# Performance work log

Hardware: AMD Instinct MI355X
Metric: run time of the kernel (lower is better)

Reference implementation:

```python
import jax, jax.numpy as jnp
import numpy as np
from jax import lax

VOCAB = 32000
EMB = 512
HID = 512
NLAYERS = 2


def _lstm_cell(x, h, c, Wih, Whh, bih, bhh):
    # x:[N,in], h,c:[N,H]; torch gate order i,f,g,o
    z = x @ Wih.T + h @ Whh.T + bih + bhh  # [N,4H]
    i, f, g, o = jnp.split(z, 4, axis=-1)
    c_new = jax.nn.sigmoid(f) * c + jax.nn.sigmoid(i) * jnp.tanh(g)
    h_new = jax.nn.sigmoid(o) * jnp.tanh(c_new)
    return h_new, c_new


def _run_encoder(x_seq, Wih, Whh, bih, bhh):
    # x_seq:[T,N,E]; stacked per-layer weights Wih:[L,4H,in], Whh:[L,4H,H]
    N = x_seq.shape[1]
    H = Whh.shape[-1]
    hs, cs = [], []
    for l in range(Wih.shape[0]):
        h0 = jnp.zeros((N, H), x_seq.dtype)
        c0 = jnp.zeros((N, H), x_seq.dtype)

        def step(carry, x, l=l):
            h, c = carry
            h, c = _lstm_cell(x, h, c, Wih[l], Whh[l], bih[l], bhh[l])
            return (h, c), h

        (hL, cL), x_seq = lax.scan(step, (h0, c0), x_seq)
        hs.append(hL)
        cs.append(cL)
    return jnp.stack(hs), jnp.stack(cs)  # [L,N,H] each


def setup_inputs() -> dict:
    key = jax.random.key(0)
    ks = jax.random.split(key, 16)
    s = 0.05
    inp = {
        "src": jax.random.randint(ks[0], (64, 64), 0, VOCAB),
        "tgt": jax.random.randint(ks[1], (32, 64), 0, VOCAB),
        "enc_emb": jax.random.normal(ks[2], (VOCAB, EMB), jnp.float32) * s,
        "enc_Wih": jax.random.normal(ks[3], (NLAYERS, 4 * HID, EMB), jnp.float32) * s,
        "enc_Whh": jax.random.normal(ks[4], (NLAYERS, 4 * HID, HID), jnp.float32) * s,
        "enc_bih": jax.random.normal(ks[5], (NLAYERS, 4 * HID), jnp.float32) * s,
        "enc_bhh": jax.random.normal(ks[6], (NLAYERS, 4 * HID), jnp.float32) * s,
        "dec_emb": jax.random.normal(ks[7], (VOCAB, EMB), jnp.float32) * s,
        "dec_Wih": jax.random.normal(ks[8], (NLAYERS, 4 * HID, EMB), jnp.float32) * s,
        "dec_Whh": jax.random.normal(ks[9], (NLAYERS, 4 * HID, HID), jnp.float32) * s,
        "dec_bih": jax.random.normal(ks[10], (NLAYERS, 4 * HID), jnp.float32) * s,
        "dec_bhh": jax.random.normal(ks[11], (NLAYERS, 4 * HID), jnp.float32) * s,
        "fc_W": jax.random.normal(ks[12], (VOCAB, HID), jnp.float32) * s,
        "fc_b": jax.random.normal(ks[13], (VOCAB,), jnp.float32) * s,
    }
    return inp


def reference(src, tgt, enc_emb, enc_Wih, enc_Whh, enc_bih, enc_bhh,
              dec_emb, dec_Wih, dec_Whh, dec_bih, dec_bhh, fc_W, fc_b):
    tgt_len, batch = tgt.shape
    # Encoder: embed src then 2-layer LSTM; final (h, c) seeds the decoder.
    src_emb = enc_emb[src]  # [T,N,E] (dropout is identity at p-eval)
    h, c = _run_encoder(src_emb, enc_Wih, enc_Whh, enc_bih, enc_bhh)

    def dec_step(carry, _):
        inp, h, c = carry  # inp:[N] int, h/c:[L,N,H]
        x = dec_emb[inp]  # [N,E]
        hs, cs = [], []
        for l in range(NLAYERS):
            hn, cn = _lstm_cell(x, h[l], c[l], dec_Wih[l], dec_Whh[l],
                                dec_bih[l], dec_bhh[l])
            hs.append(hn)
            cs.append(cn)
            x = hn
        pred = x @ fc_W.T + fc_b  # [N,V]
        nxt = jnp.argmax(pred, axis=-1)  # greedy feedback (ratio=0)
        return (nxt, jnp.stack(hs), jnp.stack(cs)), pred

    init = (tgt[0], h, c)
    _, preds = lax.scan(dec_step, init, None, length=tgt_len - 1)  # [T-1,N,V]
    outputs = jnp.concatenate(
        [jnp.zeros((1, batch, fc_W.shape[0]), preds.dtype), preds], axis=0)
    return outputs[None]  # [B=1, tgt_len, batch, vocab]
```

## Files before the change

kernel.cpp:

```cpp
#include <hip/hip_runtime.h>
#include <cmath>

#define NBLK 256
#define NTHR 512
#define SMEM_BYTES 137216

struct Args {
  const int* src; const int* tgt;
  const float* enc_emb;
  const float* enc_Wih; const float* enc_Whh; const float* enc_bih; const float* enc_bhh;
  const float* dec_emb;
  const float* dec_Wih; const float* dec_Whh; const float* dec_bih; const float* dec_bhh;
  const float* fc_W; const float* fc_b;
  float* out;
  unsigned* bar;
  unsigned long long* gkeys;
  float* hT0[2]; float* hT1[2];
  float* hnm;
  float* seqT;
  float* fcWT;
  int use_wt;
};

__device__ __forceinline__ void gbar(unsigned* bar) {
  __syncthreads();
  if (threadIdx.x == 0) {
    unsigned* gen = bar + 128;
    unsigned g = __hip_atomic_load(gen, __ATOMIC_RELAXED, __HIP_MEMORY_SCOPE_AGENT);
    __hip_atomic_fetch_add(bar + (blockIdx.x & 7) * 16, 1u, __ATOMIC_RELEASE,
                           __HIP_MEMORY_SCOPE_AGENT);
    if (blockIdx.x == 0) {
      unsigned long long target = (unsigned long long)(g + 1) * NBLK;
      for (;;) {
        unsigned long long tot = 0;
#pragma unroll
        for (int i = 0; i < 8; ++i)
          tot += __hip_atomic_load(bar + i * 16, __ATOMIC_RELAXED,
                                   __HIP_MEMORY_SCOPE_AGENT);
        if (tot >= target) break;
      }
      __builtin_amdgcn_fence(__ATOMIC_ACQUIRE, "agent");
      __hip_atomic_fetch_add(gen, 1u, __ATOMIC_RELEASE, __HIP_MEMORY_SCOPE_AGENT);
    } else {
      while (__hip_atomic_load(gen, __ATOMIC_RELAXED, __HIP_MEMORY_SCOPE_AGENT) == g)
        __builtin_amdgcn_s_sleep(1);
      __builtin_amdgcn_fence(__ATOMIC_ACQUIRE, "agent");
    }
  }
  __syncthreads();
}

__device__ __forceinline__ float sigm(float x) { return 1.f / (1.f + expf(-x)); }

__device__ __forceinline__ unsigned long long packkey(float v, int j) {
  unsigned u = __float_as_uint(v);
  u = (u & 0x80000000u) ? ~u : (u | 0x80000000u);
  return ((unsigned long long)u << 32) |
         (unsigned long long)(0xFFFFFFFFu - (unsigned)j);
}

__device__ __forceinline__ unsigned long long umaxll(unsigned long long a,
                                                     unsigned long long b) {
  return a > b ? a : b;
}

__device__ __forceinline__ void fma4(float x, float4 w, float* acc) {
  acc[0] = fmaf(x, w.x, acc[0]); acc[1] = fmaf(x, w.y, acc[1]);
  acc[2] = fmaf(x, w.z, acc[2]); acc[3] = fmaf(x, w.w, acc[3]);
}

__device__ void load_w(float* wlds, float* blds, int rbase,
                       const float* __restrict__ Wih, const float* __restrict__ Whh,
                       const float* __restrict__ bih, const float* __restrict__ bhh)
{
  const int tid = threadIdx.x, bid = blockIdx.x;
  for (int idx = tid; idx < 8 * 256; idx += NTHR) {
    const int r = idx >> 8, c = idx & 255;
    const int j = (r >> 1) * 512 + bid * 2 + (r & 1);
    float4 v;
    if (c < 128) v = *(const float4*)(Wih + (size_t)j * 512 + c * 4);
    else         v = *(const float4*)(Whh + (size_t)j * 512 + (c - 128) * 4);
    *(float4*)(wlds + (size_t)(rbase + r) * 1024 + c * 4) = v;
  }
  if (tid < 8) {
    const int j = (tid >> 1) * 512 + bid * 2 + (tid & 1);
    blds[rbase + tid] = bih[j] + bhh[j];
  }
}

__device__ void fill_tok(unsigned* toklds, const int* __restrict__ idx,
                         const unsigned long long* __restrict__ gkeys)
{
  if (threadIdx.x < 64) {
    unsigned row;
    if (idx) {
      row = (unsigned)idx[threadIdx.x];
    } else {
      unsigned long long best = gkeys[threadIdx.x];
#pragma unroll
      for (int i = 1; i < 8; ++i) best = umaxll(best, gkeys[i * 64 + threadIdx.x]);
      row = 0xFFFFFFFFu - (unsigned)best;
    }
    toklds[threadIdx.x] = row;
  }
  __syncthreads();
}

__device__ void cell(int gather, const float* __restrict__ xsrc,
                     const float* __restrict__ hT_rd, float* __restrict__ hT_wr,
                     int wrow0, float* __restrict__ cl,
                     float* __restrict__ seqT_out, float* __restrict__ hnm_out,
                     const float* __restrict__ wlds, const float* __restrict__ blds,
                     float* __restrict__ tiles, float* __restrict__ zbuf,
                     const unsigned* __restrict__ toklds)
{
  const int tid = threadIdx.x;
  const int lane = tid & 63, wv = tid >> 6;
  const int gate = wv & 3, kh = wv >> 2;
  const int r0 = gate * 2, r1 = r0 + 1;
  const float* wb0 = wlds + (size_t)(wrow0 + r0) * 1024 + kh * 512;
  const float* wb1 = wlds + (size_t)(wrow0 + r1) * 1024 + kh * 512;
  float a0 = 0.f, a1 = 0.f, e0 = 0.f, e1 = 0.f;
  float4 rg0, rg1, rg2, rg3;

  auto load_iter = [&](int it) {
    if (gather) {
      unsigned row = toklds[lane];
      const float* er = xsrc + (size_t)row * 512 + it * 64 + wv * 8;
      rg0 = *(const float4*)er;
      rg1 = *(const float4*)(er + 4);
      const float* hs = hT_rd + it * 4096 + wv * 512 + lane * 4;
      rg2 = *(const float4*)hs;
      rg3 = *(const float4*)(hs + 256);
    } else {
      const float* s = (wv < 4) ? (xsrc + it * 4096 + wv * 1024 + lane * 4)
                                : (hT_rd + it * 4096 + (wv - 4) * 1024 + lane * 4);
      rg0 = *(const float4*)s;
      rg1 = *(const float4*)(s + 256);
      rg2 = *(const float4*)(s + 512);
      rg3 = *(const float4*)(s + 768);
    }
  };
  auto commit_iter = [&](int buf) {
    float* tb = tiles + buf * 8192;
    if (gather) {
      float* tx = tb + (wv * 8) * 64 + lane;
      tx[0]   = rg0.x; tx[64]  = rg0.y; tx[128] = rg0.z; tx[192] = rg0.w;
      tx[256] = rg1.x; tx[320] = rg1.y; tx[384] = rg1.z; tx[448] = rg1.w;
      float* th = tb + 4096 + wv * 512 + lane * 4;
      *(float4*)th = rg2;
      *(float4*)(th + 256) = rg3;
    } else {
      float* t0 = tb + wv * 1024 + lane * 4;
      *(float4*)t0 = rg0;
      *(float4*)(t0 + 256) = rg1;
      *(float4*)(t0 + 512) = rg2;
      *(float4*)(t0 + 768) = rg3;
    }
  };

  load_iter(0);
  commit_iter(0);
#pragma unroll 1
  for (int it = 0; it < 8; ++it) {
    __syncthreads();
    if (it < 7) load_iter(it + 1);
    const float* w0 = wb0 + it * 64;
    const float* w1 = wb1 + it * 64;
    const float* tp = tiles + (it & 1) * 8192 + kh * 4096 + lane;
#pragma unroll
    for (int kk = 0; kk < 64; kk += 4) {
      float4 c0 = *(const float4*)(w0 + kk);
      float4 c1 = *(const float4*)(w1 + kk);
      float x0 = tp[(kk + 0) * 64], x1 = tp[(kk + 1) * 64];
      float x2 = tp[(kk + 2) * 64], x3 = tp[(kk + 3) * 64];
      a0 = fmaf(x0, c0.x, a0); e0 = fmaf(x1, c0.y, e0);
      a0 = fmaf(x2, c0.z, a0); e0 = fmaf(x3, c0.w, e0);
      a1 = fmaf(x0, c1.x, a1); e1 = fmaf(x1, c1.y, e1);
      a1 = fmaf(x2, c1.z, a1); e1 = fmaf(x3, c1.w, e1);
    }
    if (it < 7) commit_iter((it + 1) & 1);
  }
  zbuf[kh * 512 + r0 * 64 + lane] = a0 + e0;
  zbuf[kh * 512 + r1 * 64 + lane] = a1 + e1;
  __syncthreads();
  if (tid < 128) {
    const int mloc = tid >> 6, n = tid & 63;
    float z[4];
#pragma unroll
    for (int g = 0; g < 4; ++g) {
      const int r = g * 2 + mloc;
      z[g] = zbuf[r * 64 + n] + zbuf[512 + r * 64 + n] + blds[wrow0 + r];
    }
    float ig = sigm(z[0]), fg = sigm(z[1]);
    float gg = tanhf(z[2]), og = sigm(z[3]);
    const int m = blockIdx.x * 2 + mloc;
    float cc = fg * cl[mloc * 64 + n] + ig * gg;
    cl[mloc * 64 + n] = cc;
    float hh = og * tanhf(cc);
    hT_wr[m * 64 + n] = hh;
    if (seqT_out) seqT_out[m * 64 + n] = hh;
    if (hnm_out) hnm_out[n * 512 + m] = hh;
  }
}

__device__ void fc_phase(unsigned long long* skeys, int d,
                         const float* __restrict__ h,
                         const float* __restrict__ fcW,
                         const float* __restrict__ fcWT, int use_wt,
                         const float* __restrict__ fcb,
                         float* __restrict__ out,
                         unsigned long long* __restrict__ gkeys, int do_arg)
{
  const int tid = threadIdx.x, bid = blockIdx.x;
  if (do_arg && tid < 64) skeys[tid] = 0ULL;
  __syncthreads();
  if (bid < 250) {
    const int jt = tid & 31, nt = tid >> 5;
    const int j0 = bid * 128 + jt * 4;
    const int n0 = nt * 4;
    float acc[4][4] = {};
    if (use_wt) {
      const float* wt = fcWT + j0;
#pragma unroll 2
      for (int k = 0; k < 512; k += 8) {
        float4 wv[8];
#pragma unroll
        for (int i = 0; i < 8; ++i)
          wv[i] = *(const float4*)(wt + (size_t)(k + i) * 32000);
        float4 ha[4], hb[4];
#pragma unroll
        for (int ni = 0; ni < 4; ++ni) {
          ha[ni] = *(const float4*)(h + (size_t)(n0 + ni) * 512 + k);
          hb[ni] = *(const float4*)(h + (size_t)(n0 + ni) * 512 + k + 4);
        }
#pragma unroll
        for (int ni = 0; ni < 4; ++ni) {
          fma4(ha[ni].x, wv[0], acc[ni]); fma4(ha[ni].y, wv[1], acc[ni]);
          fma4(ha[ni].z, wv[2], acc[ni]); fma4(ha[ni].w, wv[3], acc[ni]);
          fma4(hb[ni].x, wv[4], acc[ni]); fma4(hb[ni].y, wv[5], acc[ni]);
          fma4(hb[ni].z, wv[6], acc[ni]); fma4(hb[ni].w, wv[7], acc[ni]);
        }
      }
    } else {
#pragma unroll 2
      for (int k = 0; k < 512; k += 8) {
        float4 wr[4][2];
#pragma unroll
        for (int i = 0; i < 4; ++i) {
          wr[i][0] = *(const float4*)(fcW + (size_t)(j0 + i) * 512 + k);
          wr[i][1] = *(const float4*)(fcW + (size_t)(j0 + i) * 512 + k + 4);
        }
        float4 ha[4], hb[4];
#pragma unroll
        for (int ni = 0; ni < 4; ++ni) {
          ha[ni] = *(const float4*)(h + (size_t)(n0 + ni) * 512 + k);
          hb[ni] = *(const float4*)(h + (size_t)(n0 + ni) * 512 + k + 4);
        }
#pragma unroll
        for (int ni = 0; ni < 4; ++ni) {
#pragma unroll
          for (int ji = 0; ji < 4; ++ji) {
            float s = acc[ni][ji];
            s = fmaf(ha[ni].x, wr[ji][0].x, s); s = fmaf(ha[ni].y, wr[ji][0].y, s);
            s = fmaf(ha[ni].z, wr[ji][0].z, s); s = fmaf(ha[ni].w, wr[ji][0].w, s);
            s = fmaf(hb[ni].x, wr[ji][1].x, s); s = fmaf(hb[ni].y, wr[ji][1].y, s);
            s = fmaf(hb[ni].z, wr[ji][1].z, s); s = fmaf(hb[ni].w, wr[ji][1].w, s);
            acc[ni][ji] = s;
          }
        }
      }
    }
    const float b0 = fcb[j0], b1 = fcb[j0 + 1], b2 = fcb[j0 + 2], b3 = fcb[j0 + 3];
#pragma unroll
    for (int ni = 0; ni < 4; ++ni) {
      const int n = n0 + ni;
      float4 v = make_float4(acc[ni][0] + b0, acc[ni][1] + b1,
                             acc[ni][2] + b2, acc[ni][3] + b3);
      *(float4*)(out + ((size_t)(d + 1) * 64 + n) * 32000 + j0) = v;
      if (do_arg) {
        unsigned long long kb = umaxll(umaxll(packkey(v.x, j0), packkey(v.y, j0 + 1)),
                                       umaxll(packkey(v.z, j0 + 2), packkey(v.w, j0 + 3)));
        atomicMax(&skeys[n], kb);
      }
    }
  }
  __syncthreads();
  if (do_arg && bid < 250 && tid < 64)
    atomicMax(&gkeys[(bid & 7) * 64 + tid], skeys[tid]);
}

__global__ void __launch_bounds__(256) fc_transpose(const float* __restrict__ W,
                                                    float* __restrict__ WT)
{
  __shared__ float tile[64][65];
  const int jb = blockIdx.x * 64;
  const int kb = blockIdx.y * 64;
  const int t = threadIdx.x;
  const int row = t >> 2, seg = t & 3;
  const float* src = W + (size_t)(jb + row) * 512 + kb + seg * 16;
#pragma unroll
  for (int i = 0; i < 4; ++i) {
    float4 v = *(const float4*)(src + i * 4);
    tile[row][seg * 16 + i * 4 + 0] = v.x;
    tile[row][seg * 16 + i * 4 + 1] = v.y;
    tile[row][seg * 16 + i * 4 + 2] = v.z;
    tile[row][seg * 16 + i * 4 + 3] = v.w;
  }
  __syncthreads();
  float* dst = WT + (size_t)(kb + row) * 32000 + jb + seg * 16;
#pragma unroll
  for (int i = 0; i < 4; ++i) {
    float4 v = make_float4(tile[seg * 16 + i * 4 + 0][row], tile[seg * 16 + i * 4 + 1][row],
                           tile[seg * 16 + i * 4 + 2][row], tile[seg * 16 + i * 4 + 3][row]);
    *(float4*)(dst + i * 4) = v;
  }
}

extern "C" __global__ void __launch_bounds__(NTHR, 2)
s2s_main(Args a)
{
  extern __shared__ float smem[];
  float* wlds  = smem;
  float* tiles = wlds + 16384;
  float* zbuf  = tiles + 16384;
  float* blds  = zbuf + 1024;
  float* clds  = blds + 16;
  unsigned* toklds = (unsigned*)(clds + 256);
  unsigned long long* skeys = (unsigned long long*)(toklds + 64);

  const int tid = threadIdx.x;

  load_w(wlds, blds, 0, a.enc_Wih, a.enc_Whh, a.enc_bih, a.enc_bhh);
  load_w(wlds, blds, 8, a.enc_Wih + (size_t)2048 * 512, a.enc_Whh + (size_t)2048 * 512,
         a.enc_bih + 2048, a.enc_bhh + 2048);
  if (tid < 256) clds[tid] = 0.f;
  __syncthreads();
  int p0 = 0, p1 = 0;
#pragma unroll 1
  for (int t = 0; t < 65; ++t) {
    if (t < 64) {
      fill_tok(toklds, a.src + t * 64, nullptr);
      cell(1, a.enc_emb, a.hT0[p0], a.hT0[p0 ^ 1], 0, clds,
           a.seqT + (size_t)t * 32768, nullptr, wlds, blds, tiles, zbuf, toklds);
      p0 ^= 1;
    }
    if (t >= 1) {
      cell(0, a.seqT + (size_t)(t - 1) * 32768, a.hT1[p1], a.hT1[p1 ^ 1], 8, clds + 128,
           nullptr, nullptr, wlds, blds, tiles, zbuf, toklds);
      p1 ^= 1;
    }
    gbar(a.bar);
  }
  load_w(wlds, blds, 0, a.dec_Wih, a.dec_Whh, a.dec_bih, a.dec_bhh);
  load_w(wlds, blds, 8, a.dec_Wih + (size_t)2048 * 512, a.dec_Whh + (size_t)2048 * 512,
         a.dec_bih + 2048, a.dec_bhh + 2048);
  __syncthreads();
#pragma unroll 1
  for (int d = 0; d < 31; ++d) {
    fill_tok(toklds, d == 0 ? a.tgt : nullptr, a.gkeys);
    cell(1, a.dec_emb, a.hT0[p0], a.hT0[p0 ^ 1], 0, clds,
         nullptr, nullptr, wlds, blds, tiles, zbuf, toklds);
    p0 ^= 1;
    gbar(a.bar);
    if (blockIdx.x == 0) a.gkeys[tid] = 0ULL;
    cell(0, a.hT0[p0], a.hT1[p1], a.hT1[p1 ^ 1], 8, clds + 128,
         nullptr, a.hnm, wlds, blds, tiles, zbuf, toklds);
    p1 ^= 1;
    gbar(a.bar);
    fc_phase(skeys, d, a.hnm, a.fc_W, a.fcWT, a.use_wt, a.fc_b, a.out, a.gkeys, d < 30);
    if (d < 30) gbar(a.bar);
  }
}

extern "C" void kernel_launch(void* const* d_in, const int* in_sizes, int n_in,
                              void* d_out, int out_size, void* d_ws, size_t ws_size,
                              hipStream_t stream)
{
  (void)in_sizes; (void)n_in; (void)out_size;
  Args a;
  a.src     = (const int*)d_in[0];
  a.tgt     = (const int*)d_in[1];
  a.enc_emb = (const float*)d_in[2];
  a.enc_Wih = (const float*)d_in[3];
  a.enc_Whh = (const float*)d_in[4];
  a.enc_bih = (const float*)d_in[5];
  a.enc_bhh = (const float*)d_in[6];
  a.dec_emb = (const float*)d_in[7];
  a.dec_Wih = (const float*)d_in[8];
  a.dec_Whh = (const float*)d_in[9];
  a.dec_bih = (const float*)d_in[10];
  a.dec_bhh = (const float*)d_in[11];
  a.fc_W    = (const float*)d_in[12];
  a.fc_b    = (const float*)d_in[13];
  a.out     = (float*)d_out;

  char* ws = (char*)d_ws;
  a.bar   = (unsigned*)ws;
  a.gkeys = (unsigned long long*)(ws + 1024);
  float* f = (float*)(ws + 8192);
  a.hT0[0] = f;
  a.hT0[1] = f + 32768;
  a.hT1[0] = f + 65536;
  a.hT1[1] = f + 98304;
  a.hnm    = f + 131072;
  a.seqT   = f + 163840;
  size_t base_f = 163840 + 2097152;
  a.fcWT = nullptr; a.use_wt = 0;
  size_t wt_need = 8192 + (base_f + (size_t)512 * 32000) * 4;
  if (ws_size >= wt_need) { a.fcWT = f + base_f; a.use_wt = 1; }

  hipFuncSetAttribute((const void*)s2s_main,
                      hipFuncAttributeMaxDynamicSharedMemorySize, SMEM_BYTES);

  hipMemsetAsync(d_ws, 0, 8192 + (size_t)131072 * 4, stream);
  hipMemsetAsync(d_out, 0, (size_t)64 * 32000 * 4, stream);
  if (a.use_wt)
    fc_transpose<<<dim3(500, 8), 256, 0, stream>>>(a.fc_W, a.fcWT);

  void* params[] = {&a};
  hipLaunchCooperativeKernel((const void*)s2s_main, dim3(NBLK), dim3(NTHR),
                             params, SMEM_BYTES, stream);
}
```

Before: 6.830 ms.

## Stream LSTM weights from global memory instead of staging them in LDS

Measured after the change: 8.406 ms. 1.23x slower.

```diff
diff --git a/kernel.cpp b/kernel.cpp
--- a/kernel.cpp
+++ b/kernel.cpp
@@ -3,7 +3,7 @@
 
 #define NBLK 256
 #define NTHR 512
-#define SMEM_BYTES 137216
+#define SMEM_BYTES 18432
 
 struct Args {
   const int* src; const int* tgt;
@@ -15,8 +15,7 @@
   float* out;
   unsigned* bar;
   unsigned long long* gkeys;
-  float* hT0[2]; float* hT1[2];
-  float* hnm;
+  float* h0[2]; float* h1[2];
   float* seqT;
   float* fcWT;
   int use_wt;
@@ -69,22 +68,12 @@
   acc[2] = fmaf(x, w.z, acc[2]); acc[3] = fmaf(x, w.w, acc[3]);
 }
 
-__device__ void load_w(float* wlds, float* blds, int rbase,
-                       const float* __restrict__ Wih, const float* __restrict__ Whh,
+__device__ void load_b(float* blds, int rbase,
                        const float* __restrict__ bih, const float* __restrict__ bhh)
 {
-  const int tid = threadIdx.x, bid = blockIdx.x;
-  for (int idx = tid; idx < 8 * 256; idx += NTHR) {
-    const int r = idx >> 8, c = idx & 255;
-    const int j = (r >> 1) * 512 + bid * 2 + (r & 1);
-    float4 v;
-    if (c < 128) v = *(const float4*)(Wih + (size_t)j * 512 + c * 4);
-    else         v = *(const float4*)(Whh + (size_t)j * 512 + (c - 128) * 4);
-    *(float4*)(wlds + (size_t)(rbase + r) * 1024 + c * 4) = v;
-  }
-  if (tid < 8) {
-    const int j = (tid >> 1) * 512 + bid * 2 + (tid & 1);
-    blds[rbase + tid] = bih[j] + bhh[j];
+  if (threadIdx.x < 8) {
+    const int j = (threadIdx.x >> 1) * 512 + blockIdx.x * 2 + (threadIdx.x & 1);
+    blds[rbase + threadIdx.x] = bih[j] + bhh[j];
   }
 }
 
@@ -107,82 +96,56 @@
 }
 
 __device__ void cell(int gather, const float* __restrict__ xsrc,
-                     const float* __restrict__ hT_rd, float* __restrict__ hT_wr,
-                     int wrow0, float* __restrict__ cl,
-                     float* __restrict__ seqT_out, float* __restrict__ hnm_out,
-                     const float* __restrict__ wlds, const float* __restrict__ blds,
-                     float* __restrict__ tiles, float* __restrict__ zbuf,
+                     const float* __restrict__ h_rd, float* __restrict__ h_wr,
+                     const float* __restrict__ Wih, const float* __restrict__ Whh,
+                     int rbase, float* __restrict__ cl,
+                     float* __restrict__ seq_out,
+                     const float* __restrict__ blds, float* __restrict__ zbuf,
                      const unsigned* __restrict__ toklds)
 {
   const int tid = threadIdx.x;
   const int lane = tid & 63, wv = tid >> 6;
-  const int gate = wv & 3, kh = wv >> 2;
-  const int r0 = gate * 2, r1 = r0 + 1;
-  const float* wb0 = wlds + (size_t)(wrow0 + r0) * 1024 + kh * 512;
-  const float* wb1 = wlds + (size_t)(wrow0 + r1) * 1024 + kh * 512;
-  float a0 = 0.f, a1 = 0.f, e0 = 0.f, e1 = 0.f;
-  float4 rg0, rg1, rg2, rg3;
-
-  auto load_iter = [&](int it) {
-    if (gather) {
-      unsigned row = toklds[lane];
-      const float* er = xsrc + (size_t)row * 512 + it * 64 + wv * 8;
-      rg0 = *(const float4*)er;
-      rg1 = *(const float4*)(er + 4);
-      const float* hs = hT_rd + it * 4096 + wv * 512 + lane * 4;
-      rg2 = *(const float4*)hs;
-      rg3 = *(const float4*)(hs + 256);
-    } else {
-      const float* s = (wv < 4) ? (xsrc + it * 4096 + wv * 1024 + lane * 4)
-                                : (hT_rd + it * 4096 + (wv - 4) * 1024 + lane * 4);
-      rg0 = *(const float4*)s;
-      rg1 = *(const float4*)(s + 256);
-      rg2 = *(const float4*)(s + 512);
-      rg3 = *(const float4*)(s + 768);
-    }
-  };
-  auto commit_iter = [&](int buf) {
-    float* tb = tiles + buf * 8192;
-    if (gather) {
-      float* tx = tb + (wv * 8) * 64 + lane;
-      tx[0]   = rg0.x; tx[64]  = rg0.y; tx[128] = rg0.z; tx[192] = rg0.w;
-      tx[256] = rg1.x; tx[320] = rg1.y; tx[384] = rg1.z; tx[448] = rg1.w;
-      float* th = tb + 4096 + wv * 512 + lane * 4;
-      *(float4*)th = rg2;
-      *(float4*)(th + 256) = rg3;
-    } else {
-      float* t0 = tb + wv * 1024 + lane * 4;
-      *(float4*)t0 = rg0;
-      *(float4*)(t0 + 256) = rg1;
-      *(float4*)(t0 + 512) = rg2;
-      *(float4*)(t0 + 768) = rg3;
-    }
-  };
-
-  load_iter(0);
-  commit_iter(0);
+  const int bid2 = blockIdx.x * 2;
+  const float* xs = gather ? xsrc + (size_t)toklds[lane] * 512
+                           : xsrc + (size_t)lane * 512;
+  const float* hs = h_rd + (size_t)lane * 512;
+
+  float acc[8] = {0.f, 0.f, 0.f, 0.f, 0.f, 0.f, 0.f, 0.f};
+  const int k0 = wv * 8;
+  float4 xa0 = *(const float4*)(xs + k0), xa1 = *(const float4*)(xs + k0 + 4);
+  float4 ha0 = *(const float4*)(hs + k0), ha1 = *(const float4*)(hs + k0 + 4);
+
 #pragma unroll 1
   for (int it = 0; it < 8; ++it) {
-    __syncthreads();
-    if (it < 7) load_iter(it + 1);
-    const float* w0 = wb0 + it * 64;
-    const float* w1 = wb1 + it * 64;
-    const float* tp = tiles + (it & 1) * 8192 + kh * 4096 + lane;
-#pragma unroll
-    for (int kk = 0; kk < 64; kk += 4) {
-      float4 c0 = *(const float4*)(w0 + kk);
-      float4 c1 = *(const float4*)(w1 + kk);
-      float x0 = tp[(kk + 0) * 64], x1 = tp[(kk + 1) * 64];
-      float x2 = tp[(kk + 2) * 64], x3 = tp[(kk + 3) * 64];
-      a0 = fmaf(x0, c0.x, a0); e0 = fmaf(x1, c0.y, e0);
-      a0 = fmaf(x2, c0.z, a0); e0 = fmaf(x3, c0.w, e0);
-      a1 = fmaf(x0, c1.x, a1); e1 = fmaf(x1, c1.y, e1);
-      a1 = fmaf(x2, c1.z, a1); e1 = fmaf(x3, c1.w, e1);
-    }
-    if (it < 7) commit_iter((it + 1) & 1);
-  }
-  zbuf[kh * 512 + r0 * 64 + lane] = a0 + e0;
-  zbuf[kh * 512 + r1 * 64 + lane] = a1 + e1;
+    const int kc = it * 64 + k0;
+    float4 xb0, xb1, hb0, hb1;
+    if (it < 7) {
+      xb0 = *(const float4*)(xs + kc + 64); xb1 = *(const float4*)(xs + kc + 68);
+      hb0 = *(const float4*)(hs + kc + 64); hb1 = *(const float4*)(hs + kc + 68);
+    }
+#pragma unroll
+    for (int r = 0; r < 8; ++r) {
+      const size_t j = (size_t)((r >> 1) * 512 + bid2 + (r & 1));
+      const float* wi = Wih + j * 512 + kc;
+      const float* wh = Whh + j * 512 + kc;
+      float4 w0 = *(const float4*)wi, w1 = *(const float4*)(wi + 4);
+      float4 u0 = *(const float4*)wh, u1 = *(const float4*)(wh + 4);
+      float s = acc[r];
+      s = fmaf(w0.x, xa0.x, s); s = fmaf(w0.y, xa0.y, s);
+      s = fmaf(w0.z, xa0.z, s); s = fmaf(w0.w, xa0.w, s);
+      s = fmaf(w1.x, xa1.x, s); s = fmaf(w1.y, xa1.y, s);
+      s = fmaf(w1.z, xa1.z, s); s = fmaf(w1.w, xa1.w, s);
+      s = fmaf(u0.x, ha0.x, s); s = fmaf(u0.y, ha0.y, s);
+      s = fmaf(u0.z, ha0.z, s); s = fmaf(u0.w, ha0.w, s);
+      s = fmaf(u1.x, ha1.x, s); s = fmaf(u1.y, ha1.y, s);
+      s = fmaf(u1.z, ha1.z, s); s = fmaf(u1.w, ha1.w, s);
+      acc[r] = s;
+    }
+    if (it < 7) { xa0 = xb0; xa1 = xb1; ha0 = hb0; ha1 = hb1; }
+  }
+#pragma unroll
+  for (int r = 0; r < 8; ++r)
+    zbuf[wv * 512 + r * 64 + lane] = acc[r];
   __syncthreads();
   if (tid < 128) {
     const int mloc = tid >> 6, n = tid & 63;
@@ -190,18 +153,21 @@
 #pragma unroll
     for (int g = 0; g < 4; ++g) {
       const int r = g * 2 + mloc;
-      z[g] = zbuf[r * 64 + n] + zbuf[512 + r * 64 + n] + blds[wrow0 + r];
+      float s = blds[rbase + r];
+#pragma unroll
+      for (int w = 0; w < 8; ++w) s += zbuf[w * 512 + r * 64 + n];
+      z[g] = s;
     }
     float ig = sigm(z[0]), fg = sigm(z[1]);
     float gg = tanhf(z[2]), og = sigm(z[3]);
-    const int m = blockIdx.x * 2 + mloc;
+    const int m = bid2 + mloc;
     float cc = fg * cl[mloc * 64 + n] + ig * gg;
     cl[mloc * 64 + n] = cc;
     float hh = og * tanhf(cc);
-    hT_wr[m * 64 + n] = hh;
-    if (seqT_out) seqT_out[m * 64 + n] = hh;
-    if (hnm_out) hnm_out[n * 512 + m] = hh;
-  }
+    h_wr[(size_t)n * 512 + m] = hh;
+    if (seq_out) seq_out[(size_t)n * 512 + m] = hh;
+  }
+  __syncthreads();
 }
 
 __device__ void fc_phase(unsigned long long* skeys, int d,
@@ -321,54 +287,53 @@
 s2s_main(Args a)
 {
   extern __shared__ float smem[];
-  float* wlds  = smem;
-  float* tiles = wlds + 16384;
-  float* zbuf  = tiles + 16384;
-  float* blds  = zbuf + 1024;
-  float* clds  = blds + 16;
+  float* zbuf = smem;
+  float* blds = zbuf + 4096;
+  float* clds = blds + 16;
   unsigned* toklds = (unsigned*)(clds + 256);
   unsigned long long* skeys = (unsigned long long*)(toklds + 64);
 
   const int tid = threadIdx.x;
 
-  load_w(wlds, blds, 0, a.enc_Wih, a.enc_Whh, a.enc_bih, a.enc_bhh);
-  load_w(wlds, blds, 8, a.enc_Wih + (size_t)2048 * 512, a.enc_Whh + (size_t)2048 * 512,
-         a.enc_bih + 2048, a.enc_bhh + 2048);
+  load_b(blds, 0, a.enc_bih, a.enc_bhh);
+  load_b(blds, 8, a.enc_bih + 2048, a.enc_bhh + 2048);
   if (tid < 256) clds[tid] = 0.f;
   __syncthreads();
+  const float* E1i = a.enc_Wih + (size_t)2048 * 512;
+  const float* E1h = a.enc_Whh + (size_t)2048 * 512;
   int p0 = 0, p1 = 0;
 #pragma unroll 1
   for (int t = 0; t < 65; ++t) {
     if (t < 64) {
       fill_tok(toklds, a.src + t * 64, nullptr);
-      cell(1, a.enc_emb, a.hT0[p0], a.hT0[p0 ^ 1], 0, clds,
-           a.seqT + (size_t)t * 32768, nullptr, wlds, blds, tiles, zbuf, toklds);
+      cell(1, a.enc_emb, a.h0[p0], a.h0[p0 ^ 1], a.enc_Wih, a.enc_Whh, 0, clds,
+           a.seqT + (size_t)t * 32768, blds, zbuf, toklds);
       p0 ^= 1;
     }
     if (t >= 1) {
-      cell(0, a.seqT + (size_t)(t - 1) * 32768, a.hT1[p1], a.hT1[p1 ^ 1], 8, clds + 128,
-           nullptr, nullptr, wlds, blds, tiles, zbuf, toklds);
+      cell(0, a.seqT + (size_t)(t - 1) * 32768, a.h1[p1], a.h1[p1 ^ 1], E1i, E1h, 8,
+           clds + 128, nullptr, blds, zbuf, toklds);
       p1 ^= 1;
     }
     gbar(a.bar);
   }
-  load_w(wlds, blds, 0, a.dec_Wih, a.dec_Whh, a.dec_bih, a.dec_bhh);
-  load_w(wlds, blds, 8, a.dec_Wih + (size_t)2048 * 512, a.dec_Whh + (size_t)2048 * 512,
-         a.dec_bih + 2048, a.dec_bhh + 2048);
-  __syncthreads();
+  load_b(blds, 0, a.dec_bih, a.dec_bhh);
+  load_b(blds, 8, a.dec_bih + 2048, a.dec_bhh + 2048);
+  const float* D1i = a.dec_Wih + (size_t)2048 * 512;
+  const float* D1h = a.dec_Whh + (size_t)2048 * 512;
 #pragma unroll 1
   for (int d = 0; d < 31; ++d) {
     fill_tok(toklds, d == 0 ? a.tgt : nullptr, a.gkeys);
-    cell(1, a.dec_emb, a.hT0[p0], a.hT0[p0 ^ 1], 0, clds,
-         nullptr, nullptr, wlds, blds, tiles, zbuf, toklds);
+    cell(1, a.dec_emb, a.h0[p0], a.h0[p0 ^ 1], a.dec_Wih, a.dec_Whh, 0, clds,
+         nullptr, blds, zbuf, toklds);
     p0 ^= 1;
     gbar(a.bar);
     if (blockIdx.x == 0) a.gkeys[tid] = 0ULL;
-    cell(0, a.hT0[p0], a.hT1[p1], a.hT1[p1 ^ 1], 8, clds + 128,
-         nullptr, a.hnm, wlds, blds, tiles, zbuf, toklds);
+    cell(0, a.h0[p0], a.h1[p1], a.h1[p1 ^ 1], D1i, D1h, 8, clds + 128,
+         nullptr, blds, zbuf, toklds);
     p1 ^= 1;
     gbar(a.bar);
-    fc_phase(skeys, d, a.hnm, a.fc_W, a.fcWT, a.use_wt, a.fc_b, a.out, a.gkeys, d < 30);
+    fc_phase(skeys, d, a.h1[p1], a.fc_W, a.fcWT, a.use_wt, a.fc_b, a.out, a.gkeys, d < 30);
     if (d < 30) gbar(a.bar);
   }
 }
@@ -399,13 +364,12 @@
   a.bar   = (unsigned*)ws;
   a.gkeys = (unsigned long long*)(ws + 1024);
   float* f = (float*)(ws + 8192);
-  a.hT0[0] = f;
-  a.hT0[1] = f + 32768;
-  a.hT1[0] = f + 65536;
-  a.hT1[1] = f + 98304;
-  a.hnm    = f + 131072;
-  a.seqT   = f + 163840;
-  size_t base_f = 163840 + 2097152;
+  a.h0[0] = f;
+  a.h0[1] = f + 32768;
+  a.h1[0] = f + 65536;
+  a.h1[1] = f + 98304;
+  a.seqT  = f + 131072;
+  size_t base_f = 131072 + 2097152;
   a.fcWT = nullptr; a.use_wt = 0;
   size_t wt_need = 8192 + (base_f + (size_t)512 * 32000) * 4;
   if (ws_size >= wt_need) { a.fcWT = f + base_f; a.use_wt = 1; }
```

## Repartition LSTM cell matvec so each wave owns a K-slice for all eight rows

Applied to the files above, without the earlier changes.

Result: faster. 6.470 ms (-5.3%).

```diff
diff --git a/kernel.cpp b/kernel.cpp
--- a/kernel.cpp
+++ b/kernel.cpp
@@ -3,7 +3,7 @@
 
 #define NBLK 256
 #define NTHR 512
-#define SMEM_BYTES 137216
+#define SMEM_BYTES 149312
 
 struct Args {
   const int* src; const int* tgt;
@@ -116,11 +116,10 @@
 {
   const int tid = threadIdx.x;
   const int lane = tid & 63, wv = tid >> 6;
-  const int gate = wv & 3, kh = wv >> 2;
-  const int r0 = gate * 2, r1 = r0 + 1;
-  const float* wb0 = wlds + (size_t)(wrow0 + r0) * 1024 + kh * 512;
-  const float* wb1 = wlds + (size_t)(wrow0 + r1) * 1024 + kh * 512;
-  float a0 = 0.f, a1 = 0.f, e0 = 0.f, e1 = 0.f;
+  const int vbase = (wv < 4) ? wv * 1024 : 4096 + (wv - 4) * 1024;
+  const int wcol0 = (wv < 4) ? wv * 16 : 512 + (wv - 4) * 16;
+  const float* wrow = wlds + (size_t)wrow0 * 1024 + wcol0;
+  float acc[8] = {0.f, 0.f, 0.f, 0.f, 0.f, 0.f, 0.f, 0.f};
   float4 rg0, rg1, rg2, rg3;
 
   auto load_iter = [&](int it) {
@@ -165,24 +164,27 @@
   for (int it = 0; it < 8; ++it) {
     __syncthreads();
     if (it < 7) load_iter(it + 1);
-    const float* w0 = wb0 + it * 64;
-    const float* w1 = wb1 + it * 64;
-    const float* tp = tiles + (it & 1) * 8192 + kh * 4096 + lane;
-#pragma unroll
-    for (int kk = 0; kk < 64; kk += 4) {
-      float4 c0 = *(const float4*)(w0 + kk);
-      float4 c1 = *(const float4*)(w1 + kk);
-      float x0 = tp[(kk + 0) * 64], x1 = tp[(kk + 1) * 64];
-      float x2 = tp[(kk + 2) * 64], x3 = tp[(kk + 3) * 64];
-      a0 = fmaf(x0, c0.x, a0); e0 = fmaf(x1, c0.y, e0);
-      a0 = fmaf(x2, c0.z, a0); e0 = fmaf(x3, c0.w, e0);
-      a1 = fmaf(x0, c1.x, a1); e1 = fmaf(x1, c1.y, e1);
-      a1 = fmaf(x2, c1.z, a1); e1 = fmaf(x3, c1.w, e1);
+    const float* tp = tiles + (it & 1) * 8192 + vbase + lane;
+    const float* wb = wrow + it * 64;
+    float val[16];
+#pragma unroll
+    for (int j = 0; j < 16; ++j) val[j] = tp[j * 64];
+#pragma unroll
+    for (int jq = 0; jq < 4; ++jq) {
+#pragma unroll
+      for (int r = 0; r < 8; ++r) {
+        float4 w = *(const float4*)(wb + r * 1024 + jq * 4);
+        float s = acc[r];
+        s = fmaf(w.x, val[jq * 4 + 0], s); s = fmaf(w.y, val[jq * 4 + 1], s);
+        s = fmaf(w.z, val[jq * 4 + 2], s); s = fmaf(w.w, val[jq * 4 + 3], s);
+        acc[r] = s;
+      }
     }
     if (it < 7) commit_iter((it + 1) & 1);
   }
-  zbuf[kh * 512 + r0 * 64 + lane] = a0 + e0;
-  zbuf[kh * 512 + r1 * 64 + lane] = a1 + e1;
+#pragma unroll
+  for (int r = 0; r < 8; ++r)
+    zbuf[wv * 512 + r * 64 + lane] = acc[r];
   __syncthreads();
   if (tid < 128) {
     const int mloc = tid >> 6, n = tid & 63;
@@ -190,7 +192,10 @@
 #pragma unroll
     for (int g = 0; g < 4; ++g) {
       const int r = g * 2 + mloc;
-      z[g] = zbuf[r * 64 + n] + zbuf[512 + r * 64 + n] + blds[wrow0 + r];
+      float s = blds[wrow0 + r];
+#pragma unroll
+      for (int w = 0; w < 8; ++w) s += zbuf[w * 512 + r * 64 + n];
+      z[g] = s;
     }
     float ig = sigm(z[0]), fg = sigm(z[1]);
     float gg = tanhf(z[2]), og = sigm(z[3]);
@@ -324,7 +329,7 @@
   float* wlds  = smem;
   float* tiles = wlds + 16384;
   float* zbuf  = tiles + 16384;
-  float* blds  = zbuf + 1024;
+  float* blds  = zbuf + 4096;
   float* clds  = blds + 16;
   unsigned* toklds = (unsigned*)(clds + 256);
   unsigned long long* skeys = (unsigned long long*)(toklds + 64);
```
